# Kernel optimization log

Hardware: AMD Instinct MI355X
Metric: run time of the kernel (lower is better)

## Reference

```python
import jax, jax.numpy as jnp
from jax import lax
import numpy as np

B, T, E, D, EMB, O, L, A = 32, 500, 1024, 1024, 256, 5000, 99, 512
IGNORE = -1


def setup_inputs() -> dict:
    key = jax.random.key(0)
    ks = jax.random.split(key, 32)
    hs_pad = jax.random.normal(ks[0], (B, T, E), jnp.float32)
    hlens = jax.random.randint(ks[1], (B,), 250, T + 1).astype(jnp.int32)
    hlens = hlens.at[0].set(T)
    ylens = jax.random.randint(ks[2], (B,), 50, L + 1)
    labels = jax.random.randint(ks[3], (B, L), 0, O - 1)
    ys_pad = jnp.where(jnp.arange(L)[None, :] < ylens[:, None], labels, IGNORE)

    def w(k, shape, fan):
        return jax.random.normal(k, shape, jnp.float32) / np.float32(np.sqrt(fan))

    params = dict(
        embed=w(ks[4], (O, EMB), EMB),
        W1_W=w(ks[5], (EMB, 2 * D), EMB), b1_W=jnp.zeros(2 * D, jnp.float32),
        W1_Wx=w(ks[6], (EMB, D), EMB), b1_Wx=jnp.zeros(D, jnp.float32),
        U1=w(ks[7], (D, 2 * D), D), Ux1=w(ks[8], (D, D), D),
        U2=w(ks[9], (D, 2 * D), D), b2=jnp.zeros(2 * D, jnp.float32),
        Wc=w(ks[10], (E, 2 * D), E),
        Ux2=w(ks[11], (D, D), D), bUx2=jnp.zeros(D, jnp.float32),
        Wcx=w(ks[12], (E, D), E),
        Winit=w(ks[13], (E, D), E), binit=jnp.zeros(D, jnp.float32),
        Ws=w(ks[14], (D, D), D), bs=jnp.zeros(D, jnp.float32),
        Wy=w(ks[15], (EMB, D), EMB),
        We=w(ks[16], (E, D), E),
        Wlogit=w(ks[17], (D // 2, O), D // 2), blogit=jnp.zeros(O, jnp.float32),
        Wenc=w(ks[18], (E, A), E), Wdec=w(ks[19], (D, A), D),
    )
    return {"hs_pad": hs_pad, "hlens": hlens, "ys_pad": ys_pad, **params}


def reference(hs_pad, hlens, ys_pad, embed, W1_W, b1_W, W1_Wx, b1_Wx, U1, Ux1,
              U2, b2, Wc, Ux2, bUx2, Wcx, Winit, binit, Ws, bs, Wy, We,
              Wlogit, blogit, Wenc, Wdec):
    b, t, e = hs_pad.shape
    d = U1.shape[0]
    o = Wlogit.shape[1]
    sos = eos = o - 1
    l = ys_pad.shape[1]
    olen = l + 1

    ylens = jnp.sum(ys_pad != IGNORE, axis=1)                       # [B]
    ys_in = jnp.concatenate(
        [jnp.full((b, 1), sos, ys_pad.dtype),
         jnp.where(ys_pad == IGNORE, eos, ys_pad)], axis=1)          # [B, olen]
    ymask = (jnp.arange(olen)[None, :] < (ylens + 1)[:, None]).astype(hs_pad.dtype)
    cmask = (jnp.arange(t)[None, :] < hlens[:, None]).astype(hs_pad.dtype)

    # mean_init_state: sums all frames (incl. padding, as in original), / hlens
    h0 = (hs_pad.sum(1) / hlens[:, None].astype(hs_pad.dtype)) @ Winit + binit
    alpha0 = cmask / (cmask.sum(1, keepdims=True) + 1e-8)

    eys = embed[ys_in]                                               # [B, olen, EMB]
    sb_ = eys @ W1_W + b1_W                                          # rnn1_W(eys)
    sbx = eys @ W1_Wx + b1_Wx                                        # rnn1_Wx(eys)

    enc_att = jnp.tanh(hs_pad @ Wenc)                                # [B,T,A] precomputed

    def step(carry, xs):
        h_, alpha = carry
        x_, xx_, m_, sb = xs
        # first GRU cell
        pre1 = jax.nn.sigmoid(h_ @ U1 + x_)
        r1, u1 = pre1[:, :d], pre1[:, d:]
        h1 = jnp.tanh((h_ @ Ux1) * r1 + xx_)
        h1 = u1 * h_ + (1.0 - u1) * h1
        h1 = m_[:, None] * h1 + (1.0 - m_)[:, None] * h_
        # masked dot attention
        dq = jnp.tanh(h1 @ Wdec)                                     # [B,A]
        en = jnp.einsum('bta,ba->bt', enc_att, dq)
        en = jnp.where(cmask > 0, en, -1e9)
        w_att = jax.nn.softmax(en, axis=1)
        c = jnp.einsum('bt,bte->be', w_att, hs_pad)                  # [B,E]
        # second (conditioned) GRU cell
        pre2 = jax.nn.sigmoid(h1 @ U2 + b2 + c @ Wc)
        r2, u2 = pre2[:, :d], pre2[:, d:]
        h2 = jnp.tanh((h1 @ Ux2 + bUx2) * r2 + c @ Wcx)
        h2 = u2 * h1 + (1.0 - u2) * h2
        h2 = m_[:, None] * h2 + (1.0 - m_)[:, None] * h1
        # maxout classifier
        logit = h2 @ Ws + bs + sb @ Wy + c @ We                      # [B,D]
        logit = logit.reshape(b, d // 2, 2).max(-1)
        probs = jax.nn.softmax(logit @ Wlogit + blogit, axis=-1)
        return (h2, w_att), probs

    xs = (jnp.swapaxes(sb_, 0, 1), jnp.swapaxes(sbx, 0, 1),
          ymask.T, jnp.swapaxes(eys, 0, 1))
    _, out = lax.scan(step, (h0, alpha0), xs)                        # [olen,B,O]
    return jnp.swapaxes(out, 0, 1)                                   # [B,olen,O]
```

## Files before the change

### kernel.cpp

```cpp
#include <hip/hip_runtime.h>
#include <math.h>

static constexpr int Bb   = 32;
static constexpr int Tt   = 500;
static constexpr int Ee   = 1024;
static constexpr int EMBc = 256;
static constexpr int Oo   = 5000;
static constexpr int Llen = 99;
static constexpr int OLEN = 100;
static constexpr int Aa   = 512;


__global__ void k_ylens(const int* __restrict__ ys, int* __restrict__ ylens) {
    int b = threadIdx.x;
    if (b < Bb) {
        int c = 0;
        for (int i = 0; i < Llen; i++) c += (ys[b * Llen + i] != -1) ? 1 : 0;
        ylens[b] = c;
    }
}

__global__ void k_embed(const int* __restrict__ ys, const float* __restrict__ embed,
                        float* __restrict__ eys) {
    int blk = blockIdx.x;
    int b = blk / OLEN, i = blk % OLEN;
    int id = Oo - 1;
    if (i > 0) {
        int v = ys[b * Llen + i - 1];
        id = (v == -1) ? (Oo - 1) : v;
    }
    eys[(size_t)(b * OLEN + i) * EMBc + threadIdx.x] = embed[(size_t)id * EMBc + threadIdx.x];
}

__global__ void k_hmean(const float* __restrict__ hs, const int* __restrict__ hlens,
                        float* __restrict__ hm) {
    int b = blockIdx.y;
    int e = blockIdx.x * 256 + threadIdx.x;
    float sum = 0.f;
    for (int t = 0; t < Tt; t++) sum += hs[((size_t)b * Tt + t) * Ee + e];
    hm[(size_t)b * Ee + e] = sum / (float)hlens[b];
}

template <int ACT>
__global__ void k_gemm_tiled(const float* __restrict__ Amat, const float* __restrict__ W,
                             const float* __restrict__ bias, float* __restrict__ C,
                             int M, int K, int N) {
    __shared__ float As[16][132];
    __shared__ float Wt[16][68];
    const int tid = threadIdx.x;
    const int row0 = blockIdx.y * 128;
    const int col0 = blockIdx.x * 64;
    const int ty = tid >> 4, tx = tid & 15;
    float acc[8][4] = {};
    for (int kk = 0; kk < K; kk += 16) {
#pragma unroll
        for (int rr = 0; rr < 128; rr += 64) {
            int r = rr + (tid >> 2);
            int c4 = (tid & 3) * 4;
            float4 v = make_float4(0.f, 0.f, 0.f, 0.f);
            if (row0 + r < M) v = *(const float4*)(&Amat[(size_t)(row0 + r) * K + kk + c4]);
            As[c4 + 0][r] = v.x; As[c4 + 1][r] = v.y; As[c4 + 2][r] = v.z; As[c4 + 3][r] = v.w;
        }
        for (int i = tid; i < 16 * 64; i += 256)
            Wt[i >> 6][i & 63] = W[(size_t)(kk + (i >> 6)) * N + col0 + (i & 63)];
        __syncthreads();
#pragma unroll
        for (int k = 0; k < 16; k++) {
            float a[8], bbv[4];
#pragma unroll
            for (int i = 0; i < 8; i++) a[i] = As[k][ty * 8 + i];
#pragma unroll
            for (int j = 0; j < 4; j++) bbv[j] = Wt[k][tx * 4 + j];
#pragma unroll
            for (int i = 0; i < 8; i++)
#pragma unroll
                for (int j = 0; j < 4; j++) acc[i][j] += a[i] * bbv[j];
        }
        __syncthreads();
    }
#pragma unroll
    for (int i = 0; i < 8; i++) {
        int r = row0 + ty * 8 + i;
        if (r < M) {
#pragma unroll
            for (int j = 0; j < 4; j++) {
                int cc = col0 + tx * 4 + j;
                float v = acc[i][j];
                if (bias) v += bias[cc];
                if (ACT == 1) v = tanhf(v);
                C[(size_t)r * N + cc] = v;
            }
        }
    }
}


template <int KC>
__global__ void k_gemm3(const float* __restrict__ x, int ldx,
                        const float* __restrict__ Wga, const float* __restrict__ Wgb,
                        const float* __restrict__ Wxa, const float* __restrict__ Wxb,
                        int kSeg, float* __restrict__ P) {
    __shared__ float xs[Bb][KC];
    const int tid = threadIdx.x;
    const int kc = blockIdx.y;
    const int k0 = kc * KC;
    for (int i = tid; i < Bb * KC; i += 256) {
        int bb = i / KC, k = i - bb * KC;
        xs[bb][k] = x[(size_t)bb * ldx + k0 + k];
    }
    __syncthreads();
    const int tx = tid & 63, ty = tid >> 6;
    const int j = blockIdx.x * 64 + tx;
    const int b0 = ty * 8;
    const bool seg0 = (k0 < kSeg);
    const float* Wg = seg0 ? Wga : Wgb;
    const float* Wx = seg0 ? Wxa : Wxb;
    const int kbase = seg0 ? k0 : (k0 - kSeg);
    float ag[8] = {}, au[8] = {}, ax[8] = {};
    for (int kk = 0; kk < KC; kk++) {
        const float* wgr = Wg + (size_t)(kbase + kk) * 2048;
        const float* wxr = Wx + (size_t)(kbase + kk) * 1024;
        float wg0 = wgr[j], wg1 = wgr[j + 1024], wx0 = wxr[j];
#pragma unroll
        for (int i = 0; i < 8; i++) {
            float xv = xs[b0 + i][kk];
            ag[i] += xv * wg0;
            au[i] += xv * wg1;
            ax[i] += xv * wx0;
        }
    }
#pragma unroll
    for (int i = 0; i < 8; i++) {
        P[(((size_t)kc * 3 + 0) * Bb + b0 + i) * 1024 + j] = ag[i];
        P[(((size_t)kc * 3 + 1) * Bb + b0 + i) * 1024 + j] = au[i];
        P[(((size_t)kc * 3 + 2) * Bb + b0 + i) * 1024 + j] = ax[i];
    }
}

template <int KC>
__global__ void k_gemm1(const float* __restrict__ x, int ldx,
                        const float* __restrict__ Wa, const float* __restrict__ Wb,
                        int kSeg, int N, float* __restrict__ P) {
    __shared__ float xs[Bb][KC];
    const int tid = threadIdx.x;
    const int kc = blockIdx.y;
    const int k0 = kc * KC;
    for (int i = tid; i < Bb * KC; i += 256) {
        int bb = i / KC, k = i - bb * KC;
        xs[bb][k] = x[(size_t)bb * ldx + k0 + k];
    }
    __syncthreads();
    const int tx = tid & 63, ty = tid >> 6;
    const int j = blockIdx.x * 64 + tx;
    const int b0 = ty * 8;
    const bool seg0 = (k0 < kSeg);
    const float* W = seg0 ? Wa : Wb;
    const int kbase = seg0 ? k0 : (k0 - kSeg);
    float acc[8] = {};
    for (int kk = 0; kk < KC; kk++) {
        float w = W[(size_t)(kbase + kk) * N + j];
#pragma unroll
        for (int i = 0; i < 8; i++) acc[i] += xs[b0 + i][kk] * w;
    }
#pragma unroll
    for (int i = 0; i < 8; i++) P[((size_t)kc * Bb + b0 + i) * N + j] = acc[i];
}

__global__ void k_comb1(const float* __restrict__ P, const float* __restrict__ sb,
                        const float* __restrict__ sbx, const float* __restrict__ h,
                        const int* __restrict__ ylens, float* __restrict__ x23, int s) {
    int gid = blockIdx.x * 256 + threadIdx.x;
    int b = gid >> 10, j = gid & 1023;
    float s0 = 0, s1 = 0, sx = 0;
#pragma unroll
    for (int kc = 0; kc < 16; kc++) {
        s0 += P[(((size_t)kc * 3 + 0) * Bb + b) * 1024 + j];
        s1 += P[(((size_t)kc * 3 + 1) * Bb + b) * 1024 + j];
        sx += P[(((size_t)kc * 3 + 2) * Bb + b) * 1024 + j];
    }
    float r = 1.f / (1.f + expf(-(s0 + sb[((size_t)b * OLEN + s) * 2048 + j])));
    float u = 1.f / (1.f + expf(-(s1 + sb[((size_t)b * OLEN + s) * 2048 + 1024 + j])));
    float ht = tanhf(sx * r + sbx[((size_t)b * OLEN + s) * 1024 + j]);
    float hp = h[(size_t)b * 1024 + j];
    float h1 = u * hp + (1.f - u) * ht;
    float m = (s < ylens[b] + 1) ? 1.f : 0.f;
    h1 = m * h1 + (1.f - m) * hp;
    x23[(size_t)b * 2048 + j] = h1;
}

__global__ void k_en(const float* __restrict__ pd, const float* __restrict__ enc,
                     float* __restrict__ en, float* __restrict__ x23) {
    __shared__ float dqs[Aa];
    const int tid = threadIdx.x;
    const int b = blockIdx.y, tt = blockIdx.x;
    if (tid < 128) x23[(size_t)b * 2048 + 1024 + tt * 128 + tid] = 0.f;
    for (int jj = tid; jj < Aa; jj += 256) {
        float sum = 0;
#pragma unroll
        for (int kc = 0; kc < 16; kc++) sum += pd[((size_t)kc * Bb + b) * Aa + jj];
        dqs[jj] = tanhf(sum);
    }
    __syncthreads();
    const int tx = tid & 63, ty = tid >> 6;
    for (int t2 = 0; t2 < 64; t2 += 4) {
        int t = tt * 64 + t2 + ty;
        if (t < Tt) {
            float acc = 0;
            const float* er = enc + ((size_t)b * Tt + t) * Aa;
#pragma unroll
            for (int i = 0; i < 8; i++) acc += er[tx + 64 * i] * dqs[tx + 64 * i];
#pragma unroll
            for (int off = 32; off > 0; off >>= 1) acc += __shfl_down(acc, off, 64);
            if (tx == 0) en[(size_t)b * 512 + t] = acc;
        }
    }
}

__global__ void k_softc(const float* __restrict__ en, const float* __restrict__ hs,
                        const int* __restrict__ hlens, float* __restrict__ x23) {
    __shared__ float wts[Tt];
    __shared__ float red[128];
    const int tid = threadIdx.x;
    const int b = blockIdx.z;
    const int hlen = hlens[b];
    float mx = -1e30f;
    for (int t = tid; t < hlen; t += 128) mx = fmaxf(mx, en[(size_t)b * 512 + t]);
    red[tid] = mx;
    __syncthreads();
    for (int w = 64; w > 0; w >>= 1) {
        if (tid < w) red[tid] = fmaxf(red[tid], red[tid + w]);
        __syncthreads();
    }
    mx = red[0];
    __syncthreads();
    float ps = 0;
    for (int t = tid; t < Tt; t += 128) {
        float w = 0.f;
        if (t < hlen) w = expf(en[(size_t)b * 512 + t] - mx);
        wts[t] = w;
        ps += w;
    }
    red[tid] = ps;
    __syncthreads();
    for (int w = 64; w > 0; w >>= 1) {
        if (tid < w) red[tid] += red[tid + w];
        __syncthreads();
    }
    float inv = 1.f / red[0];
    __syncthreads();
    for (int t = tid; t < Tt; t += 128) wts[t] *= inv;
    __syncthreads();

    const int e0 = blockIdx.x * 512 + tid * 4;
    const int tc = blockIdx.y;
    int tstart = tc * 125;
    int tend = tstart + 125;
    if (tend > hlen) tend = hlen;
    float4 a0 = make_float4(0, 0, 0, 0), a1 = make_float4(0, 0, 0, 0);
    float4 a2 = make_float4(0, 0, 0, 0), a3 = make_float4(0, 0, 0, 0);
    int t = tstart;
    for (; t + 3 < tend; t += 4) {
        float w0 = wts[t], w1 = wts[t + 1], w2 = wts[t + 2], w3 = wts[t + 3];
        float4 h0 = *(const float4*)(&hs[((size_t)b * Tt + t) * Ee + e0]);
        float4 h1 = *(const float4*)(&hs[((size_t)b * Tt + t + 1) * Ee + e0]);
        float4 h2 = *(const float4*)(&hs[((size_t)b * Tt + t + 2) * Ee + e0]);
        float4 h3 = *(const float4*)(&hs[((size_t)b * Tt + t + 3) * Ee + e0]);
        a0.x += w0 * h0.x; a0.y += w0 * h0.y; a0.z += w0 * h0.z; a0.w += w0 * h0.w;
        a1.x += w1 * h1.x; a1.y += w1 * h1.y; a1.z += w1 * h1.z; a1.w += w1 * h1.w;
        a2.x += w2 * h2.x; a2.y += w2 * h2.y; a2.z += w2 * h2.z; a2.w += w2 * h2.w;
        a3.x += w3 * h3.x; a3.y += w3 * h3.y; a3.z += w3 * h3.z; a3.w += w3 * h3.w;
    }
    for (; t < tend; t++) {
        float w = wts[t];
        float4 hv = *(const float4*)(&hs[((size_t)b * Tt + t) * Ee + e0]);
        a0.x += w * hv.x; a0.y += w * hv.y; a0.z += w * hv.z; a0.w += w * hv.w;
    }
    a0.x += a1.x + a2.x + a3.x;
    a0.y += a1.y + a2.y + a3.y;
    a0.z += a1.z + a2.z + a3.z;
    a0.w += a1.w + a2.w + a3.w;
    float* cdst = &x23[(size_t)b * 2048 + 1024 + e0];
    atomicAdd(cdst + 0, a0.x);
    atomicAdd(cdst + 1, a0.y);
    atomicAdd(cdst + 2, a0.z);
    atomicAdd(cdst + 3, a0.w);
}

__global__ void k_comb2(const float* __restrict__ P, const float* __restrict__ b2,
                        const float* __restrict__ bUx2, const int* __restrict__ ylens,
                        float* __restrict__ x23, float* __restrict__ h, int s) {
    int gid = blockIdx.x * 256 + threadIdx.x;
    int b = gid >> 10, j = gid & 1023;
    float s0 = 0, s1 = 0, xa = 0, xb = 0;
#pragma unroll
    for (int kc = 0; kc < 16; kc++) {
        s0 += P[(((size_t)kc * 3 + 0) * Bb + b) * 1024 + j];
        s1 += P[(((size_t)kc * 3 + 1) * Bb + b) * 1024 + j];
        float px = P[(((size_t)kc * 3 + 2) * Bb + b) * 1024 + j];
        if (kc < 8) xa += px; else xb += px;
    }
    float r = 1.f / (1.f + expf(-(s0 + b2[j])));
    float u = 1.f / (1.f + expf(-(s1 + b2[1024 + j])));
    float h2t = tanhf((xa + bUx2[j]) * r + xb);
    float h1v = x23[(size_t)b * 2048 + j];
    float h2 = u * h1v + (1.f - u) * h2t;
    float m = (s < ylens[b] + 1) ? 1.f : 0.f;
    h2 = m * h2 + (1.f - m) * h1v;
    x23[(size_t)b * 2048 + j] = h2;
    h[(size_t)b * 1024 + j] = h2;
}


__global__ void k_gemmL(const float* __restrict__ x23a, const float* __restrict__ eys,
                        const float* __restrict__ Ws, const float* __restrict__ We,
                        const float* __restrict__ Wy, const float* __restrict__ bs,
                        float* __restrict__ mo) {
    __shared__ float As[16][132];
    __shared__ float Wt[16][68];
    const int tid = threadIdx.x;
    const int row0 = blockIdx.y * 128;
    const int col0 = blockIdx.x * 64;
    const int ty = tid >> 4, tx = tid & 15;
    float acc[8][4] = {};
    for (int kk = 0; kk < 2304; kk += 16) {
#pragma unroll
        for (int rr = 0; rr < 128; rr += 64) {
            int rl = rr + (tid >> 2);
            int r = row0 + rl;
            int c4 = (tid & 3) * 4;
            float4 v;
            if (kk < 2048) {
                v = *(const float4*)(&x23a[(size_t)r * 2048 + kk + c4]);
            } else {
                int bI = r & 31, sI = r >> 5;
                v = *(const float4*)(&eys[((size_t)bI * OLEN + sI) * EMBc + (kk - 2048) + c4]);
            }
            As[c4 + 0][rl] = v.x; As[c4 + 1][rl] = v.y; As[c4 + 2][rl] = v.z; As[c4 + 3][rl] = v.w;
        }
        for (int i = tid; i < 16 * 64; i += 256) {
            int rowk = kk + (i >> 6);
            const float* wr = (rowk < 1024) ? &Ws[(size_t)rowk * 1024]
                             : (rowk < 2048) ? &We[(size_t)(rowk - 1024) * 1024]
                                             : &Wy[(size_t)(rowk - 2048) * 1024];
            Wt[i >> 6][i & 63] = wr[col0 + (i & 63)];
        }
        __syncthreads();
#pragma unroll
        for (int k = 0; k < 16; k++) {
            float a[8], bbv[4];
#pragma unroll
            for (int i = 0; i < 8; i++) a[i] = As[k][ty * 8 + i];
#pragma unroll
            for (int j = 0; j < 4; j++) bbv[j] = Wt[k][tx * 4 + j];
#pragma unroll
            for (int i = 0; i < 8; i++)
#pragma unroll
                for (int j = 0; j < 4; j++) acc[i][j] += a[i] * bbv[j];
        }
        __syncthreads();
    }
#pragma unroll
    for (int i = 0; i < 8; i++) {
        int r = row0 + ty * 8 + i;
#pragma unroll
        for (int p = 0; p < 2; p++) {
            int c = col0 + tx * 4 + p * 2;
            float v0 = acc[i][p * 2 + 0] + bs[c + 0];
            float v1 = acc[i][p * 2 + 1] + bs[c + 1];
            mo[(size_t)r * 512 + (c >> 1)] = fmaxf(v0, v1);
        }
    }
}

__global__ void k_gemmZ(const float* __restrict__ mo, const float* __restrict__ Wl,
                        const float* __restrict__ bl, float* __restrict__ out) {
    __shared__ float As[16][132];
    __shared__ float Wt[16][68];
    const int tid = threadIdx.x;
    const int row0 = blockIdx.y * 128;
    const int col0 = blockIdx.x * 64;
    const int ty = tid >> 4, tx = tid & 15;
    float acc[8][4] = {};
    for (int kk = 0; kk < 512; kk += 16) {
#pragma unroll
        for (int rr = 0; rr < 128; rr += 64) {
            int rl = rr + (tid >> 2);
            int r = row0 + rl;
            int c4 = (tid & 3) * 4;
            float4 v = *(const float4*)(&mo[(size_t)r * 512 + kk + c4]);
            As[c4 + 0][rl] = v.x; As[c4 + 1][rl] = v.y; As[c4 + 2][rl] = v.z; As[c4 + 3][rl] = v.w;
        }
        for (int i = tid; i < 16 * 64; i += 256) {
            int c = col0 + (i & 63);
            if (c > Oo - 1) c = Oo - 1;
            Wt[i >> 6][i & 63] = Wl[(size_t)(kk + (i >> 6)) * Oo + c];
        }
        __syncthreads();
#pragma unroll
        for (int k = 0; k < 16; k++) {
            float a[8], bbv[4];
#pragma unroll
            for (int i = 0; i < 8; i++) a[i] = As[k][ty * 8 + i];
#pragma unroll
            for (int j = 0; j < 4; j++) bbv[j] = Wt[k][tx * 4 + j];
#pragma unroll
            for (int i = 0; i < 8; i++)
#pragma unroll
                for (int j = 0; j < 4; j++) acc[i][j] += a[i] * bbv[j];
        }
        __syncthreads();
    }
#pragma unroll
    for (int i = 0; i < 8; i++) {
        int r = row0 + ty * 8 + i;
        int bI = r & 31, sI = r >> 5;
        float* zr = out + ((size_t)bI * OLEN + sI) * Oo;
#pragma unroll
        for (int j = 0; j < 4; j++) {
            int c = col0 + tx * 4 + j;
            if (c < Oo) zr[c] = acc[i][j] + bl[c];
        }
    }
}

__global__ void k_osm(float* __restrict__ out) {
    __shared__ float red[256];
    __shared__ float ev[Oo];
    const int tid = threadIdx.x;
    const int r = blockIdx.x;
    const int bI = r & 31, sI = r >> 5;
    float* zr = out + ((size_t)bI * OLEN + sI) * Oo;
    float mx = -1e30f;
    for (int i = tid; i < Oo; i += 256) mx = fmaxf(mx, zr[i]);
    red[tid] = mx;
    __syncthreads();
    for (int w = 128; w > 0; w >>= 1) {
        if (tid < w) red[tid] = fmaxf(red[tid], red[tid + w]);
        __syncthreads();
    }
    mx = red[0];
    __syncthreads();
    float ps = 0;
    for (int i = tid; i < Oo; i += 256) {
        float e = expf(zr[i] - mx);
        ev[i] = e;
        ps += e;
    }
    red[tid] = ps;
    __syncthreads();
    for (int w = 128; w > 0; w >>= 1) {
        if (tid < w) red[tid] += red[tid + w];
        __syncthreads();
    }
    float inv = 1.f / red[0];
    for (int i = tid; i < Oo; i += 256) zr[i] = ev[i] * inv;
}


extern "C" void kernel_launch(void* const* d_in, const int* in_sizes, int n_in,
                              void* d_out, int out_size, void* d_ws, size_t ws_size,
                              hipStream_t stream) {
    const float* hs    = (const float*)d_in[0];
    const int*   hlens = (const int*)d_in[1];
    const int*   ys    = (const int*)d_in[2];
    const float* embed = (const float*)d_in[3];
    const float* W1_W  = (const float*)d_in[4];
    const float* b1_W  = (const float*)d_in[5];
    const float* W1_Wx = (const float*)d_in[6];
    const float* b1_Wx = (const float*)d_in[7];
    const float* U1    = (const float*)d_in[8];
    const float* Ux1   = (const float*)d_in[9];
    const float* U2    = (const float*)d_in[10];
    const float* b2    = (const float*)d_in[11];
    const float* Wc    = (const float*)d_in[12];
    const float* Ux2   = (const float*)d_in[13];
    const float* bUx2  = (const float*)d_in[14];
    const float* Wcx   = (const float*)d_in[15];
    const float* Winit = (const float*)d_in[16];
    const float* binit = (const float*)d_in[17];
    const float* Ws    = (const float*)d_in[18];
    const float* bs    = (const float*)d_in[19];
    const float* Wy    = (const float*)d_in[20];
    const float* We    = (const float*)d_in[21];
    const float* Wlog  = (const float*)d_in[22];
    const float* blog  = (const float*)d_in[23];
    const float* Wenc  = (const float*)d_in[24];
    const float* Wdec  = (const float*)d_in[25];
    float* out = (float*)d_out;
    float* wsp = (float*)d_ws;

    float* enc_att = wsp;
    float* sb      = enc_att + (size_t)Bb * Tt * Aa;
    float* sbx     = sb      + (size_t)Bb * OLEN * 2048;
    float* eys     = sbx     + (size_t)Bb * OLEN * 1024;
    float* h       = eys     + (size_t)Bb * OLEN * EMBc;
    float* en      = h       + (size_t)Bb * 1024;
    float* pd      = en      + (size_t)Bb * 512;
    float* p3      = pd      + (size_t)16 * Bb * 512;
    int*   ylens   = (int*)(p3 + (size_t)16 * 3 * Bb * 1024);
    float* hm      = pd;
    float* mo      = pd;
    float* xall    = out;

    k_ylens<<<1, 64, 0, stream>>>(ys, ylens);
    k_embed<<<Bb * OLEN, EMBc, 0, stream>>>(ys, embed, eys);
    k_hmean<<<dim3(4, Bb), 256, 0, stream>>>(hs, hlens, hm);
    k_gemm_tiled<0><<<dim3(16, 1), 256, 0, stream>>>(hm, Winit, binit, h, Bb, 1024, 1024);
    k_gemm_tiled<0><<<dim3(32, 25), 256, 0, stream>>>(eys, W1_W, b1_W, sb, Bb * OLEN, EMBc, 2048);
    k_gemm_tiled<0><<<dim3(16, 25), 256, 0, stream>>>(eys, W1_Wx, b1_Wx, sbx, Bb * OLEN, EMBc, 1024);
    k_gemm_tiled<1><<<dim3(8, 125), 256, 0, stream>>>(hs, Wenc, nullptr, enc_att, Bb * Tt, Ee, Aa);

    for (int s = 0; s < OLEN; s++) {
        float* x23s = xall + (size_t)s * Bb * 2048;
        k_gemm3<64><<<dim3(16, 16), 256, 0, stream>>>(h, 1024, U1, U1, Ux1, Ux1, 1024, p3);
        k_comb1<<<128, 256, 0, stream>>>(p3, sb, sbx, h, ylens, x23s, s);
        k_gemm1<64><<<dim3(8, 16), 256, 0, stream>>>(x23s, 2048, Wdec, Wdec, 1024, 512, pd);
        k_en<<<dim3(8, Bb), 256, 0, stream>>>(pd, enc_att, en, x23s);
        k_softc<<<dim3(2, 4, Bb), 128, 0, stream>>>(en, hs, hlens, x23s);
        k_gemm3<128><<<dim3(16, 16), 256, 0, stream>>>(x23s, 2048, U2, Wc, Ux2, Wcx, 1024, p3);
        k_comb2<<<128, 256, 0, stream>>>(p3, b2, bUx2, ylens, x23s, h, s);
    }

    k_gemmL<<<dim3(16, 25), 256, 0, stream>>>(xall, eys, Ws, We, Wy, bs, mo);
    k_gemmZ<<<dim3(79, 25), 256, 0, stream>>>(mo, Wlog, blog, out);
    k_osm<<<Bb * OLEN, 256, 0, stream>>>(out);
}
```

Measured before the change: 12.54 ms.

## Fuse GRU combine steps into following GEMM prologues and widen GEMM tiles

Removes the standalone k_comb1 and k_comb2 kernels from the per-step loop. Their gate math now runs inside the shared-memory load phase of the next matvec kernel: the cell-2 combine moves into the next step's cell-1 GEMM, and the cell-1 combine moves into the Wdec GEMM. A tail kernel finishes the last step. This cuts two launches per decode step, at the cost of each column block re-reducing the split-K partials for its chunk (redundant L2 traffic). Separately, the tiled GEMMs (init, embedding projections, encoder attention, logit and output layers) move from 128x64 to 128x128 tiles with float4 weight loads to get more reuse per thread.

```diff
diff --git a/kernel.cpp b/kernel.cpp
--- a/kernel.cpp
+++ b/kernel.cpp
@@ -42,39 +42,45 @@
 }
 
 template <int ACT>
-__global__ void k_gemm_tiled(const float* __restrict__ Amat, const float* __restrict__ W,
-                             const float* __restrict__ bias, float* __restrict__ C,
-                             int M, int K, int N) {
+__global__ __launch_bounds__(256) void k_gemm128(const float* __restrict__ A,
+                                                 const float* __restrict__ W,
+                                                 const float* __restrict__ bias,
+                                                 float* __restrict__ C,
+                                                 int M, int K, int N) {
     __shared__ float As[16][132];
-    __shared__ float Wt[16][68];
-    const int tid = threadIdx.x;
-    const int row0 = blockIdx.y * 128;
-    const int col0 = blockIdx.x * 64;
+    __shared__ float Bs[16][132];
+    const int tid = threadIdx.x;
+    const int row0 = blockIdx.y * 128, col0 = blockIdx.x * 128;
     const int ty = tid >> 4, tx = tid & 15;
-    float acc[8][4] = {};
+    float acc[8][8] = {};
     for (int kk = 0; kk < K; kk += 16) {
 #pragma unroll
-        for (int rr = 0; rr < 128; rr += 64) {
-            int r = rr + (tid >> 2);
-            int c4 = (tid & 3) * 4;
+        for (int l = 0; l < 2; l++) {
+            int idx = tid + l * 256;
+            int r = idx >> 2, c4 = (idx & 3) * 4;
             float4 v = make_float4(0.f, 0.f, 0.f, 0.f);
-            if (row0 + r < M) v = *(const float4*)(&Amat[(size_t)(row0 + r) * K + kk + c4]);
+            if (row0 + r < M) v = *(const float4*)(&A[(size_t)(row0 + r) * K + kk + c4]);
             As[c4 + 0][r] = v.x; As[c4 + 1][r] = v.y; As[c4 + 2][r] = v.z; As[c4 + 3][r] = v.w;
         }
-        for (int i = tid; i < 16 * 64; i += 256)
-            Wt[i >> 6][i & 63] = W[(size_t)(kk + (i >> 6)) * N + col0 + (i & 63)];
+#pragma unroll
+        for (int l = 0; l < 2; l++) {
+            int idx = tid + l * 256;
+            int r = idx >> 5, c4 = (idx & 31) * 4;
+            float4 v = *(const float4*)(&W[(size_t)(kk + r) * N + col0 + c4]);
+            Bs[r][c4 + 0] = v.x; Bs[r][c4 + 1] = v.y; Bs[r][c4 + 2] = v.z; Bs[r][c4 + 3] = v.w;
+        }
         __syncthreads();
 #pragma unroll
         for (int k = 0; k < 16; k++) {
-            float a[8], bbv[4];
+            float a[8], b[8];
 #pragma unroll
             for (int i = 0; i < 8; i++) a[i] = As[k][ty * 8 + i];
 #pragma unroll
-            for (int j = 0; j < 4; j++) bbv[j] = Wt[k][tx * 4 + j];
+            for (int j = 0; j < 8; j++) b[j] = Bs[k][tx * 8 + j];
 #pragma unroll
             for (int i = 0; i < 8; i++)
 #pragma unroll
-                for (int j = 0; j < 4; j++) acc[i][j] += a[i] * bbv[j];
+                for (int j = 0; j < 8; j++) acc[i][j] += a[i] * b[j];
         }
         __syncthreads();
     }
@@ -83,47 +89,72 @@
         int r = row0 + ty * 8 + i;
         if (r < M) {
 #pragma unroll
-            for (int j = 0; j < 4; j++) {
-                int cc = col0 + tx * 4 + j;
+            for (int j = 0; j < 8; j++) {
+                int c = col0 + tx * 8 + j;
                 float v = acc[i][j];
-                if (bias) v += bias[cc];
+                if (bias) v += bias[c];
                 if (ACT == 1) v = tanhf(v);
-                C[(size_t)r * N + cc] = v;
+                C[(size_t)r * N + c] = v;
             }
         }
     }
 }
 
 
-template <int KC>
-__global__ void k_gemm3(const float* __restrict__ x, int ldx,
-                        const float* __restrict__ Wga, const float* __restrict__ Wgb,
-                        const float* __restrict__ Wxa, const float* __restrict__ Wxb,
-                        int kSeg, float* __restrict__ P) {
-    __shared__ float xs[Bb][KC];
-    const int tid = threadIdx.x;
-    const int kc = blockIdx.y;
-    const int k0 = kc * KC;
-    for (int i = tid; i < Bb * KC; i += 256) {
-        int bb = i / KC, k = i - bb * KC;
-        xs[bb][k] = x[(size_t)bb * ldx + k0 + k];
+__global__ __launch_bounds__(256) void k_cell1(
+    const float* __restrict__ hDirect, int useDirect,
+    const float* __restrict__ p3b, const float* __restrict__ h1buf,
+    const float* __restrict__ b2, const float* __restrict__ bUx2,
+    const int* __restrict__ ylens, int sPrev,
+    const float* __restrict__ U1, const float* __restrict__ Ux1,
+    float* __restrict__ p3a, float* __restrict__ hOut, float* __restrict__ x23prev) {
+    __shared__ float xs[Bb * 64];
+    const int tid = threadIdx.x;
+    const int jb = blockIdx.x, kc = blockIdx.y;
+    const int k0 = kc * 64;
+    if (useDirect) {
+        for (int i = tid; i < Bb * 64; i += 256) {
+            int bb = i >> 6, kk = i & 63;
+            xs[i] = hDirect[(size_t)bb * 1024 + k0 + kk];
+        }
+    } else {
+        for (int i = tid; i < Bb * 64; i += 256) {
+            int bb = i >> 6, kk = i & 63;
+            int j = k0 + kk;
+            float s0 = 0, s1 = 0, xa = 0, xb = 0;
+#pragma unroll
+            for (int kc2 = 0; kc2 < 16; kc2++) {
+                s0 += p3b[(((size_t)kc2 * 3 + 0) * Bb + bb) * 1024 + j];
+                s1 += p3b[(((size_t)kc2 * 3 + 1) * Bb + bb) * 1024 + j];
+                float px = p3b[(((size_t)kc2 * 3 + 2) * Bb + bb) * 1024 + j];
+                if (kc2 < 8) xa += px; else xb += px;
+            }
+            float r = 1.f / (1.f + expf(-(s0 + b2[j])));
+            float u = 1.f / (1.f + expf(-(s1 + b2[1024 + j])));
+            float h2t = tanhf((xa + bUx2[j]) * r + xb);
+            float h1v = h1buf[(size_t)bb * 1024 + j];
+            float h2 = u * h1v + (1.f - u) * h2t;
+            float m = (sPrev < ylens[bb] + 1) ? 1.f : 0.f;
+            h2 = m * h2 + (1.f - m) * h1v;
+            xs[i] = h2;
+            if (jb == 0) {
+                hOut[(size_t)bb * 1024 + j] = h2;
+                x23prev[(size_t)bb * 2048 + j] = h2;
+            }
+        }
     }
     __syncthreads();
     const int tx = tid & 63, ty = tid >> 6;
-    const int j = blockIdx.x * 64 + tx;
+    const int j = jb * 64 + tx;
     const int b0 = ty * 8;
-    const bool seg0 = (k0 < kSeg);
-    const float* Wg = seg0 ? Wga : Wgb;
-    const float* Wx = seg0 ? Wxa : Wxb;
-    const int kbase = seg0 ? k0 : (k0 - kSeg);
     float ag[8] = {}, au[8] = {}, ax[8] = {};
-    for (int kk = 0; kk < KC; kk++) {
-        const float* wgr = Wg + (size_t)(kbase + kk) * 2048;
-        const float* wxr = Wx + (size_t)(kbase + kk) * 1024;
+    for (int kk = 0; kk < 64; kk++) {
+        const float* wgr = U1 + (size_t)(k0 + kk) * 2048;
+        const float* wxr = Ux1 + (size_t)(k0 + kk) * 1024;
         float wg0 = wgr[j], wg1 = wgr[j + 1024], wx0 = wxr[j];
 #pragma unroll
         for (int i = 0; i < 8; i++) {
-            float xv = xs[b0 + i][kk];
+            float xv = xs[(b0 + i) * 64 + kk];
             ag[i] += xv * wg0;
             au[i] += xv * wg1;
             ax[i] += xv * wx0;
@@ -131,69 +162,61 @@
     }
 #pragma unroll
     for (int i = 0; i < 8; i++) {
-        P[(((size_t)kc * 3 + 0) * Bb + b0 + i) * 1024 + j] = ag[i];
-        P[(((size_t)kc * 3 + 1) * Bb + b0 + i) * 1024 + j] = au[i];
-        P[(((size_t)kc * 3 + 2) * Bb + b0 + i) * 1024 + j] = ax[i];
-    }
-}
-
-template <int KC>
-__global__ void k_gemm1(const float* __restrict__ x, int ldx,
-                        const float* __restrict__ Wa, const float* __restrict__ Wb,
-                        int kSeg, int N, float* __restrict__ P) {
-    __shared__ float xs[Bb][KC];
-    const int tid = threadIdx.x;
-    const int kc = blockIdx.y;
-    const int k0 = kc * KC;
-    for (int i = tid; i < Bb * KC; i += 256) {
-        int bb = i / KC, k = i - bb * KC;
-        xs[bb][k] = x[(size_t)bb * ldx + k0 + k];
+        p3a[(((size_t)kc * 3 + 0) * Bb + b0 + i) * 1024 + j] = ag[i];
+        p3a[(((size_t)kc * 3 + 1) * Bb + b0 + i) * 1024 + j] = au[i];
+        p3a[(((size_t)kc * 3 + 2) * Bb + b0 + i) * 1024 + j] = ax[i];
+    }
+}
+
+__global__ __launch_bounds__(256) void k_dq(
+    const float* __restrict__ p3a, const float* __restrict__ sb,
+    const float* __restrict__ sbx, const float* __restrict__ h,
+    const int* __restrict__ ylens, int s,
+    const float* __restrict__ Wdec, float* __restrict__ pd, float* __restrict__ h1buf) {
+    __shared__ float xs[Bb * 64];
+    const int tid = threadIdx.x;
+    const int jb = blockIdx.x, kc = blockIdx.y;
+    const int k0 = kc * 64;
+    for (int i = tid; i < Bb * 64; i += 256) {
+        int bb = i >> 6, kk = i & 63;
+        int j = k0 + kk;
+        float s0 = 0, s1 = 0, sx = 0;
+#pragma unroll
+        for (int kc2 = 0; kc2 < 16; kc2++) {
+            s0 += p3a[(((size_t)kc2 * 3 + 0) * Bb + bb) * 1024 + j];
+            s1 += p3a[(((size_t)kc2 * 3 + 1) * Bb + bb) * 1024 + j];
+            sx += p3a[(((size_t)kc2 * 3 + 2) * Bb + bb) * 1024 + j];
+        }
+        float r = 1.f / (1.f + expf(-(s0 + sb[((size_t)bb * OLEN + s) * 2048 + j])));
+        float u = 1.f / (1.f + expf(-(s1 + sb[((size_t)bb * OLEN + s) * 2048 + 1024 + j])));
+        float ht = tanhf(sx * r + sbx[((size_t)bb * OLEN + s) * 1024 + j]);
+        float hp = h[(size_t)bb * 1024 + j];
+        float h1 = u * hp + (1.f - u) * ht;
+        float m = (s < ylens[bb] + 1) ? 1.f : 0.f;
+        h1 = m * h1 + (1.f - m) * hp;
+        xs[i] = h1;
+        if (jb == 0) h1buf[(size_t)bb * 1024 + j] = h1;
     }
     __syncthreads();
     const int tx = tid & 63, ty = tid >> 6;
-    const int j = blockIdx.x * 64 + tx;
+    const int j = jb * 64 + tx;
     const int b0 = ty * 8;
-    const bool seg0 = (k0 < kSeg);
-    const float* W = seg0 ? Wa : Wb;
-    const int kbase = seg0 ? k0 : (k0 - kSeg);
     float acc[8] = {};
-    for (int kk = 0; kk < KC; kk++) {
-        float w = W[(size_t)(kbase + kk) * N + j];
-#pragma unroll
-        for (int i = 0; i < 8; i++) acc[i] += xs[b0 + i][kk] * w;
-    }
-#pragma unroll
-    for (int i = 0; i < 8; i++) P[((size_t)kc * Bb + b0 + i) * N + j] = acc[i];
-}
-
-__global__ void k_comb1(const float* __restrict__ P, const float* __restrict__ sb,
-                        const float* __restrict__ sbx, const float* __restrict__ h,
-                        const int* __restrict__ ylens, float* __restrict__ x23, int s) {
-    int gid = blockIdx.x * 256 + threadIdx.x;
-    int b = gid >> 10, j = gid & 1023;
-    float s0 = 0, s1 = 0, sx = 0;
-#pragma unroll
-    for (int kc = 0; kc < 16; kc++) {
-        s0 += P[(((size_t)kc * 3 + 0) * Bb + b) * 1024 + j];
-        s1 += P[(((size_t)kc * 3 + 1) * Bb + b) * 1024 + j];
-        sx += P[(((size_t)kc * 3 + 2) * Bb + b) * 1024 + j];
-    }
-    float r = 1.f / (1.f + expf(-(s0 + sb[((size_t)b * OLEN + s) * 2048 + j])));
-    float u = 1.f / (1.f + expf(-(s1 + sb[((size_t)b * OLEN + s) * 2048 + 1024 + j])));
-    float ht = tanhf(sx * r + sbx[((size_t)b * OLEN + s) * 1024 + j]);
-    float hp = h[(size_t)b * 1024 + j];
-    float h1 = u * hp + (1.f - u) * ht;
-    float m = (s < ylens[b] + 1) ? 1.f : 0.f;
-    h1 = m * h1 + (1.f - m) * hp;
-    x23[(size_t)b * 2048 + j] = h1;
+    for (int kk = 0; kk < 64; kk++) {
+        float w = Wdec[(size_t)(k0 + kk) * 512 + j];
+#pragma unroll
+        for (int i = 0; i < 8; i++) acc[i] += xs[(b0 + i) * 64 + kk] * w;
+    }
+#pragma unroll
+    for (int i = 0; i < 8; i++) pd[((size_t)kc * Bb + b0 + i) * 512 + j] = acc[i];
 }
 
 __global__ void k_en(const float* __restrict__ pd, const float* __restrict__ enc,
-                     float* __restrict__ en, float* __restrict__ x23) {
+                     float* __restrict__ en, float* __restrict__ cbuf) {
     __shared__ float dqs[Aa];
     const int tid = threadIdx.x;
     const int b = blockIdx.y, tt = blockIdx.x;
-    if (tid < 128) x23[(size_t)b * 2048 + 1024 + tt * 128 + tid] = 0.f;
+    if (tid < 128) cbuf[(size_t)b * 1024 + tt * 128 + tid] = 0.f;
     for (int jj = tid; jj < Aa; jj += 256) {
         float sum = 0;
 #pragma unroll
@@ -217,7 +240,7 @@
 }
 
 __global__ void k_softc(const float* __restrict__ en, const float* __restrict__ hs,
-                        const int* __restrict__ hlens, float* __restrict__ x23) {
+                        const int* __restrict__ hlens, float* __restrict__ cbuf) {
     __shared__ float wts[Tt];
     __shared__ float red[128];
     const int tid = threadIdx.x;
@@ -279,55 +302,101 @@
     a0.y += a1.y + a2.y + a3.y;
     a0.z += a1.z + a2.z + a3.z;
     a0.w += a1.w + a2.w + a3.w;
-    float* cdst = &x23[(size_t)b * 2048 + 1024 + e0];
+    float* cdst = &cbuf[(size_t)b * 1024 + e0];
     atomicAdd(cdst + 0, a0.x);
     atomicAdd(cdst + 1, a0.y);
     atomicAdd(cdst + 2, a0.z);
     atomicAdd(cdst + 3, a0.w);
 }
 
-__global__ void k_comb2(const float* __restrict__ P, const float* __restrict__ b2,
-                        const float* __restrict__ bUx2, const int* __restrict__ ylens,
-                        float* __restrict__ x23, float* __restrict__ h, int s) {
+__global__ __launch_bounds__(256) void k_cell2(
+    const float* __restrict__ h1buf, const float* __restrict__ cbuf,
+    const float* __restrict__ U2, const float* __restrict__ Wc,
+    const float* __restrict__ Ux2, const float* __restrict__ Wcx,
+    float* __restrict__ p3b, float* __restrict__ x23s) {
+    __shared__ float xs[Bb * 128];
+    const int tid = threadIdx.x;
+    const int jb = blockIdx.x, kc = blockIdx.y;
+    const int k0 = kc * 128;
+    const bool seg0 = (kc < 8);
+    for (int i = tid; i < Bb * 128; i += 256) {
+        int bb = i >> 7, k = i & 127;
+        float v = seg0 ? h1buf[(size_t)bb * 1024 + k0 + k]
+                       : cbuf[(size_t)bb * 1024 + (k0 - 1024) + k];
+        xs[i] = v;
+        if (!seg0 && jb == 0) x23s[(size_t)bb * 2048 + 1024 + (k0 - 1024) + k] = v;
+    }
+    __syncthreads();
+    const int tx = tid & 63, ty = tid >> 6;
+    const int j = jb * 64 + tx;
+    const int b0 = ty * 8;
+    const float* Wg = seg0 ? U2 : Wc;
+    const float* Wx = seg0 ? Ux2 : Wcx;
+    const int kbase = seg0 ? k0 : (k0 - 1024);
+    float ag[8] = {}, au[8] = {}, ax[8] = {};
+    for (int kk = 0; kk < 128; kk++) {
+        const float* wgr = Wg + (size_t)(kbase + kk) * 2048;
+        const float* wxr = Wx + (size_t)(kbase + kk) * 1024;
+        float wg0 = wgr[j], wg1 = wgr[j + 1024], wx0 = wxr[j];
+#pragma unroll
+        for (int i = 0; i < 8; i++) {
+            float xv = xs[(b0 + i) * 128 + kk];
+            ag[i] += xv * wg0;
+            au[i] += xv * wg1;
+            ax[i] += xv * wx0;
+        }
+    }
+#pragma unroll
+    for (int i = 0; i < 8; i++) {
+        p3b[(((size_t)kc * 3 + 0) * Bb + b0 + i) * 1024 + j] = ag[i];
+        p3b[(((size_t)kc * 3 + 1) * Bb + b0 + i) * 1024 + j] = au[i];
+        p3b[(((size_t)kc * 3 + 2) * Bb + b0 + i) * 1024 + j] = ax[i];
+    }
+}
+
+__global__ void k_final(const float* __restrict__ p3b, const float* __restrict__ h1buf,
+                        const float* __restrict__ b2, const float* __restrict__ bUx2,
+                        const int* __restrict__ ylens, float* __restrict__ x23last) {
     int gid = blockIdx.x * 256 + threadIdx.x;
     int b = gid >> 10, j = gid & 1023;
     float s0 = 0, s1 = 0, xa = 0, xb = 0;
 #pragma unroll
     for (int kc = 0; kc < 16; kc++) {
-        s0 += P[(((size_t)kc * 3 + 0) * Bb + b) * 1024 + j];
-        s1 += P[(((size_t)kc * 3 + 1) * Bb + b) * 1024 + j];
-        float px = P[(((size_t)kc * 3 + 2) * Bb + b) * 1024 + j];
+        s0 += p3b[(((size_t)kc * 3 + 0) * Bb + b) * 1024 + j];
+        s1 += p3b[(((size_t)kc * 3 + 1) * Bb + b) * 1024 + j];
+        float px = p3b[(((size_t)kc * 3 + 2) * Bb + b) * 1024 + j];
         if (kc < 8) xa += px; else xb += px;
     }
     float r = 1.f / (1.f + expf(-(s0 + b2[j])));
     float u = 1.f / (1.f + expf(-(s1 + b2[1024 + j])));
     float h2t = tanhf((xa + bUx2[j]) * r + xb);
-    float h1v = x23[(size_t)b * 2048 + j];
+    float h1v = h1buf[(size_t)b * 1024 + j];
     float h2 = u * h1v + (1.f - u) * h2t;
-    float m = (s < ylens[b] + 1) ? 1.f : 0.f;
+    float m = (99 < ylens[b] + 1) ? 1.f : 0.f;
     h2 = m * h2 + (1.f - m) * h1v;
-    x23[(size_t)b * 2048 + j] = h2;
-    h[(size_t)b * 1024 + j] = h2;
-}
-
-
-__global__ void k_gemmL(const float* __restrict__ x23a, const float* __restrict__ eys,
-                        const float* __restrict__ Ws, const float* __restrict__ We,
-                        const float* __restrict__ Wy, const float* __restrict__ bs,
-                        float* __restrict__ mo) {
+    x23last[(size_t)b * 2048 + j] = h2;
+}
+
+
+__global__ __launch_bounds__(256) void k_gemmL(const float* __restrict__ x23a,
+                                               const float* __restrict__ eys,
+                                               const float* __restrict__ Ws,
+                                               const float* __restrict__ We,
+                                               const float* __restrict__ Wy,
+                                               const float* __restrict__ bs,
+                                               float* __restrict__ mo) {
     __shared__ float As[16][132];
-    __shared__ float Wt[16][68];
-    const int tid = threadIdx.x;
-    const int row0 = blockIdx.y * 128;
-    const int col0 = blockIdx.x * 64;
+    __shared__ float Bs[16][132];
+    const int tid = threadIdx.x;
+    const int row0 = blockIdx.y * 128, col0 = blockIdx.x * 128;
     const int ty = tid >> 4, tx = tid & 15;
-    float acc[8][4] = {};
+    float acc[8][8] = {};
     for (int kk = 0; kk < 2304; kk += 16) {
 #pragma unroll
-        for (int rr = 0; rr < 128; rr += 64) {
-            int rl = rr + (tid >> 2);
-            int r = row0 + rl;
-            int c4 = (tid & 3) * 4;
+        for (int l = 0; l < 2; l++) {
+            int idx = tid + l * 256;
+            int r = row0 + (idx >> 2);
+            int c4 = (idx & 3) * 4;
             float4 v;
             if (kk < 2048) {
                 v = *(const float4*)(&x23a[(size_t)r * 2048 + kk + c4]);
@@ -335,27 +404,32 @@
                 int bI = r & 31, sI = r >> 5;
                 v = *(const float4*)(&eys[((size_t)bI * OLEN + sI) * EMBc + (kk - 2048) + c4]);
             }
+            int rl = idx >> 2;
             As[c4 + 0][rl] = v.x; As[c4 + 1][rl] = v.y; As[c4 + 2][rl] = v.z; As[c4 + 3][rl] = v.w;
         }
-        for (int i = tid; i < 16 * 64; i += 256) {
-            int rowk = kk + (i >> 6);
+#pragma unroll
+        for (int l = 0; l < 2; l++) {
+            int idx = tid + l * 256;
+            int r = idx >> 5, c4 = (idx & 31) * 4;
+            int rowk = kk + r;
             const float* wr = (rowk < 1024) ? &Ws[(size_t)rowk * 1024]
                              : (rowk < 2048) ? &We[(size_t)(rowk - 1024) * 1024]
                                              : &Wy[(size_t)(rowk - 2048) * 1024];
-            Wt[i >> 6][i & 63] = wr[col0 + (i & 63)];
+            float4 v = *(const float4*)(&wr[col0 + c4]);
+            Bs[r][c4 + 0] = v.x; Bs[r][c4 + 1] = v.y; Bs[r][c4 + 2] = v.z; Bs[r][c4 + 3] = v.w;
         }
         __syncthreads();
 #pragma unroll
         for (int k = 0; k < 16; k++) {
-            float a[8], bbv[4];
+            float a[8], b[8];
 #pragma unroll
             for (int i = 0; i < 8; i++) a[i] = As[k][ty * 8 + i];
 #pragma unroll
-            for (int j = 0; j < 4; j++) bbv[j] = Wt[k][tx * 4 + j];
+            for (int j = 0; j < 8; j++) b[j] = Bs[k][tx * 8 + j];
 #pragma unroll
             for (int i = 0; i < 8; i++)
 #pragma unroll
-                for (int j = 0; j < 4; j++) acc[i][j] += a[i] * bbv[j];
+                for (int j = 0; j < 8; j++) acc[i][j] += a[i] * b[j];
         }
         __syncthreads();
     }
@@ -363,50 +437,61 @@
     for (int i = 0; i < 8; i++) {
         int r = row0 + ty * 8 + i;
 #pragma unroll
-        for (int p = 0; p < 2; p++) {
-            int c = col0 + tx * 4 + p * 2;
-            float v0 = acc[i][p * 2 + 0] + bs[c + 0];
-            float v1 = acc[i][p * 2 + 1] + bs[c + 1];
+        for (int j = 0; j < 8; j += 2) {
+            int c = col0 + tx * 8 + j;
+            float v0 = acc[i][j + 0] + bs[c + 0];
+            float v1 = acc[i][j + 1] + bs[c + 1];
             mo[(size_t)r * 512 + (c >> 1)] = fmaxf(v0, v1);
         }
     }
 }
 
-__global__ void k_gemmZ(const float* __restrict__ mo, const float* __restrict__ Wl,
-                        const float* __restrict__ bl, float* __restrict__ out) {
+__global__ __launch_bounds__(256) void k_gemmZ(const float* __restrict__ mo,
+                                               const float* __restrict__ Wl,
+                                               const float* __restrict__ bl,
+                                               float* __restrict__ out) {
     __shared__ float As[16][132];
-    __shared__ float Wt[16][68];
-    const int tid = threadIdx.x;
-    const int row0 = blockIdx.y * 128;
-    const int col0 = blockIdx.x * 64;
+    __shared__ float Bs[16][132];
+    const int tid = threadIdx.x;
+    const int row0 = blockIdx.y * 128, col0 = blockIdx.x * 128;
     const int ty = tid >> 4, tx = tid & 15;
-    float acc[8][4] = {};
+    float acc[8][8] = {};
     for (int kk = 0; kk < 512; kk += 16) {
 #pragma unroll
-        for (int rr = 0; rr < 128; rr += 64) {
-            int rl = rr + (tid >> 2);
-            int r = row0 + rl;
-            int c4 = (tid & 3) * 4;
-            float4 v = *(const float4*)(&mo[(size_t)r * 512 + kk + c4]);
+        for (int l = 0; l < 2; l++) {
+            int idx = tid + l * 256;
+            int rl = idx >> 2, c4 = (idx & 3) * 4;
+            float4 v = *(const float4*)(&mo[(size_t)(row0 + rl) * 512 + kk + c4]);
             As[c4 + 0][rl] = v.x; As[c4 + 1][rl] = v.y; As[c4 + 2][rl] = v.z; As[c4 + 3][rl] = v.w;
         }
-        for (int i = tid; i < 16 * 64; i += 256) {
-            int c = col0 + (i & 63);
-            if (c > Oo - 1) c = Oo - 1;
-            Wt[i >> 6][i & 63] = Wl[(size_t)(kk + (i >> 6)) * Oo + c];
+#pragma unroll
+        for (int l = 0; l < 2; l++) {
+            int idx = tid + l * 256;
+            int r = idx >> 5, c4 = (idx & 31) * 4;
+            int cb = col0 + c4;
+            if (cb + 3 < Oo) {
+                float4 v = *(const float4*)(&Wl[(size_t)(kk + r) * Oo + cb]);
+                Bs[r][c4 + 0] = v.x; Bs[r][c4 + 1] = v.y; Bs[r][c4 + 2] = v.z; Bs[r][c4 + 3] = v.w;
+            } else {
+#pragma unroll
+                for (int q = 0; q < 4; q++) {
+                    int c = cb + q; if (c > Oo - 1) c = Oo - 1;
+                    Bs[r][c4 + q] = Wl[(size_t)(kk + r) * Oo + c];
+                }
+            }
         }
         __syncthreads();
 #pragma unroll
         for (int k = 0; k < 16; k++) {
-            float a[8], bbv[4];
+            float a[8], b[8];
 #pragma unroll
             for (int i = 0; i < 8; i++) a[i] = As[k][ty * 8 + i];
 #pragma unroll
-            for (int j = 0; j < 4; j++) bbv[j] = Wt[k][tx * 4 + j];
+            for (int j = 0; j < 8; j++) b[j] = Bs[k][tx * 8 + j];
 #pragma unroll
             for (int i = 0; i < 8; i++)
 #pragma unroll
-                for (int j = 0; j < 4; j++) acc[i][j] += a[i] * bbv[j];
+                for (int j = 0; j < 8; j++) acc[i][j] += a[i] * b[j];
         }
         __syncthreads();
     }
@@ -416,8 +501,8 @@
         int bI = r & 31, sI = r >> 5;
         float* zr = out + ((size_t)bI * OLEN + sI) * Oo;
 #pragma unroll
-        for (int j = 0; j < 4; j++) {
-            int c = col0 + tx * 4 + j;
+        for (int j = 0; j < 8; j++) {
+            int c = col0 + tx * 8 + j;
             if (c < Oo) zr[c] = acc[i][j] + bl[c];
         }
     }
@@ -494,34 +579,40 @@
     float* sbx     = sb      + (size_t)Bb * OLEN * 2048;
     float* eys     = sbx     + (size_t)Bb * OLEN * 1024;
     float* h       = eys     + (size_t)Bb * OLEN * EMBc;
-    float* en      = h       + (size_t)Bb * 1024;
+    float* h1buf   = h       + (size_t)Bb * 1024;
+    float* cbuf    = h1buf   + (size_t)Bb * 1024;
+    float* en      = cbuf    + (size_t)Bb * 1024;
     float* pd      = en      + (size_t)Bb * 512;
-    float* p3      = pd      + (size_t)16 * Bb * 512;
-    int*   ylens   = (int*)(p3 + (size_t)16 * 3 * Bb * 1024);
+    float* p3a     = pd      + (size_t)16 * Bb * 512;
+    float* p3b     = p3a     + (size_t)16 * 3 * Bb * 1024;
+    int*   ylens   = (int*)(p3b + (size_t)16 * 3 * Bb * 1024);
     float* hm      = pd;
-    float* mo      = pd;
+    float* mo      = p3a;
     float* xall    = out;
 
     k_ylens<<<1, 64, 0, stream>>>(ys, ylens);
     k_embed<<<Bb * OLEN, EMBc, 0, stream>>>(ys, embed, eys);
     k_hmean<<<dim3(4, Bb), 256, 0, stream>>>(hs, hlens, hm);
-    k_gemm_tiled<0><<<dim3(16, 1), 256, 0, stream>>>(hm, Winit, binit, h, Bb, 1024, 1024);
-    k_gemm_tiled<0><<<dim3(32, 25), 256, 0, stream>>>(eys, W1_W, b1_W, sb, Bb * OLEN, EMBc, 2048);
-    k_gemm_tiled<0><<<dim3(16, 25), 256, 0, stream>>>(eys, W1_Wx, b1_Wx, sbx, Bb * OLEN, EMBc, 1024);
-    k_gemm_tiled<1><<<dim3(8, 125), 256, 0, stream>>>(hs, Wenc, nullptr, enc_att, Bb * Tt, Ee, Aa);
+    k_gemm128<0><<<dim3(8, 1), 256, 0, stream>>>(hm, Winit, binit, h, Bb, 1024, 1024);
+    k_gemm128<0><<<dim3(16, 25), 256, 0, stream>>>(eys, W1_W, b1_W, sb, Bb * OLEN, EMBc, 2048);
+    k_gemm128<0><<<dim3(8, 25), 256, 0, stream>>>(eys, W1_Wx, b1_Wx, sbx, Bb * OLEN, EMBc, 1024);
+    k_gemm128<1><<<dim3(4, 125), 256, 0, stream>>>(hs, Wenc, nullptr, enc_att, Bb * Tt, Ee, Aa);
 
     for (int s = 0; s < OLEN; s++) {
         float* x23s = xall + (size_t)s * Bb * 2048;
-        k_gemm3<64><<<dim3(16, 16), 256, 0, stream>>>(h, 1024, U1, U1, Ux1, Ux1, 1024, p3);
-        k_comb1<<<128, 256, 0, stream>>>(p3, sb, sbx, h, ylens, x23s, s);
-        k_gemm1<64><<<dim3(8, 16), 256, 0, stream>>>(x23s, 2048, Wdec, Wdec, 1024, 512, pd);
-        k_en<<<dim3(8, Bb), 256, 0, stream>>>(pd, enc_att, en, x23s);
-        k_softc<<<dim3(2, 4, Bb), 128, 0, stream>>>(en, hs, hlens, x23s);
-        k_gemm3<128><<<dim3(16, 16), 256, 0, stream>>>(x23s, 2048, U2, Wc, Ux2, Wcx, 1024, p3);
-        k_comb2<<<128, 256, 0, stream>>>(p3, b2, bUx2, ylens, x23s, h, s);
-    }
-
-    k_gemmL<<<dim3(16, 25), 256, 0, stream>>>(xall, eys, Ws, We, Wy, bs, mo);
-    k_gemmZ<<<dim3(79, 25), 256, 0, stream>>>(mo, Wlog, blog, out);
+        float* x23prev = (s == 0) ? xall : (xall + (size_t)(s - 1) * Bb * 2048);
+        k_cell1<<<dim3(16, 16), 256, 0, stream>>>(h, (s == 0) ? 1 : 0, p3b, h1buf,
+                                                  b2, bUx2, ylens, s - 1, U1, Ux1,
+                                                  p3a, h, x23prev);
+        k_dq<<<dim3(8, 16), 256, 0, stream>>>(p3a, sb, sbx, h, ylens, s, Wdec, pd, h1buf);
+        k_en<<<dim3(8, Bb), 256, 0, stream>>>(pd, enc_att, en, cbuf);
+        k_softc<<<dim3(2, 4, Bb), 128, 0, stream>>>(en, hs, hlens, cbuf);
+        k_cell2<<<dim3(16, 16), 256, 0, stream>>>(h1buf, cbuf, U2, Wc, Ux2, Wcx, p3b, x23s);
+    }
+    k_final<<<128, 256, 0, stream>>>(p3b, h1buf, b2, bUx2, ylens,
+                                     xall + (size_t)99 * Bb * 2048);
+
+    k_gemmL<<<dim3(8, 25), 256, 0, stream>>>(xall, eys, Ws, We, Wy, bs, mo);
+    k_gemmZ<<<dim3(40, 25), 256, 0, stream>>>(mo, Wlog, blog, out);
     k_osm<<<Bb * OLEN, 256, 0, stream>>>(out);
 }
```

Measured after the change: 12.11 ms. 1.04x faster.
